# Kernel tuning notes

Hardware: AMD Instinct MI355X
Metric: run time of the kernel (lower is better)

## Reference

```python
import jax, jax.numpy as jnp
import numpy as np
from jax import lax

UNITS, FILTERS, KERNEL = 128, 32, 31
LSTM_SIZE = 1024


def _lstm_step(x, h, c, W, U, b):
    # Keras LSTMCell: gates ordered i, f, g(candidate), o
    z = x @ W + h @ U + b
    i, f, g, o = jnp.split(z, 4, axis=-1)
    c_new = jax.nn.sigmoid(f) * c + jax.nn.sigmoid(i) * jnp.tanh(g)
    h_new = jax.nn.sigmoid(o) * jnp.tanh(c_new)
    return h_new, c_new


def setup_inputs() -> dict:
    key = jax.random.key(0)
    ks = jax.random.split(key, 16)
    B, T_ENC, ENC_D = 32, 400, 512
    T_DEC, DEC_D = 800, 80
    s = 0.05
    inp = {
        "encoder_out_seq": jax.random.normal(ks[0], (B, T_ENC, ENC_D), jnp.float32),
        "decoder_out_seq": jax.random.normal(ks[1], (B, T_DEC, DEC_D), jnp.float32),
        # attention projections
        "Wm": jax.random.normal(ks[2], (ENC_D, UNITS), jnp.float32) * s,      # memory_layer
        "Wq": jax.random.normal(ks[3], (LSTM_SIZE, UNITS), jnp.float32) * s,  # query_layer
        "conv_k": jax.random.normal(ks[4], (KERNEL, 1, FILTERS), jnp.float32) * s,
        "conv_b": jnp.zeros((FILTERS,), jnp.float32),
        "Wloc": jax.random.normal(ks[5], (FILTERS, UNITS), jnp.float32) * s,  # location_layer
        "v_a": jax.random.normal(ks[6], (UNITS,), jnp.float32) * s,
        "b_a": jax.random.normal(ks[7], (UNITS,), jnp.float32) * s,
        # 2-layer decoder LSTM; layer0 input = dec_dim + enc_dim
        "W0": jax.random.normal(ks[8], (DEC_D + ENC_D, 4 * LSTM_SIZE), jnp.float32) * s,
        "U0": jax.random.normal(ks[9], (LSTM_SIZE, 4 * LSTM_SIZE), jnp.float32) * s,
        "b0": jnp.zeros((4 * LSTM_SIZE,), jnp.float32),
        "W1": jax.random.normal(ks[10], (LSTM_SIZE, 4 * LSTM_SIZE), jnp.float32) * s,
        "U1": jax.random.normal(ks[11], (LSTM_SIZE, 4 * LSTM_SIZE), jnp.float32) * s,
        "b1": jnp.zeros((4 * LSTM_SIZE,), jnp.float32),
    }
    return inp


def reference(encoder_out_seq, decoder_out_seq, Wm, Wq, conv_k, conv_b, Wloc,
              v_a, b_a, W0, U0, b0, W1, U1, b1):
    values = encoder_out_seq                      # [B, T_enc, D]
    keys = values @ Wm                            # [B, T_enc, units]
    B, T_enc, _ = values.shape

    def loc_conv(align):  # align: [B, T_enc]
        x = align[..., None]                      # [B, T_enc, 1]
        f = lax.conv_general_dilated(
            x, conv_k, window_strides=(1,), padding="SAME",
            dimension_numbers=("NWC", "WIO", "NWC"))
        return f + conv_b                         # [B, T_enc, filters]

    def step(carry, query):
        prev_align, c_i, h0, c0, h1, c1 = carry
        x = jnp.concatenate([query, c_i], axis=-1)           # [B, dec+enc]
        h0, c0 = _lstm_step(x, h0, c0, W0, U0, b0)
        h1, c1 = _lstm_step(h0, h1, c1, W1, U1, b1)
        pq = h1 @ Wq                                          # [B, units]
        loc = loc_conv(prev_align) @ Wloc                     # [B, T_enc, units]
        e = jnp.sum(v_a * jnp.tanh(keys + pq[:, None, :] + loc + b_a), axis=-1)
        a = jax.nn.softmax(e, axis=-1)                        # [B, T_enc]
        next_align = a + prev_align                           # cumulative
        c_new = jnp.einsum("bt,btd->bd", a, values)           # context
        return (next_align, c_new, h0, c0, h1, c1), a

    z = jnp.zeros
    init = (z((B, T_enc)), z((B, values.shape[-1])),
            z((B, LSTM_SIZE)), z((B, LSTM_SIZE)),
            z((B, LSTM_SIZE)), z((B, LSTM_SIZE)))
    queries = jnp.swapaxes(decoder_out_seq, 0, 1)             # [T_dec, B, dec_dim]
    _, e_tm = lax.scan(step, init, queries)                   # [T_dec, B, T_enc]
    e_outputs = jnp.swapaxes(e_tm, 0, 1)                      # [B, T_dec, T_enc]
    c_outputs = jnp.einsum("bqt,btd->bqd", e_outputs, values) # [B, T_dec, D]
    return c_outputs, e_outputs
```

## Files before the change

### kernel.cpp

```cpp
#include <hip/hip_runtime.h>
#include <hip/hip_bf16.h>
#include <math.h>
#include <stddef.h>

#define B   32
#define TE  400
#define TD  800
#define ED  512
#define DD  80
#define LS  1024
#define G4  4096
#define UN  128
#define FLT 32
#define KW  31
#define KSPLIT 16

__device__ __forceinline__ float fsig(float x){ return 1.f/(1.f+__expf(-x)); }
__device__ __forceinline__ float ftanh(float x){ return 1.f - 2.f/(__expf(2.f*x)+1.f); }

__global__ void keys_kernel(const float* __restrict__ values, const float* __restrict__ Wm,
                            float* __restrict__ keys)
{
    int b  = blockIdx.x;
    int tg = blockIdx.y;
    int tid = threadIdx.x;
    __shared__ __align__(16) float v[8*512];
    const float* vb = values + (size_t)b*TE*ED + (size_t)tg*8*ED;
    for (int i = tid; i < 8*512; i += 128) v[i] = vb[i];
    __syncthreads();
    int u = tid;
    float acc[8];
#pragma unroll
    for (int i=0;i<8;i++) acc[i]=0.f;
    for (int k=0;k<ED;k++){
        float w = Wm[k*UN + u];
#pragma unroll
        for (int tt=0; tt<8; tt++) acc[tt] += v[tt*512 + k]*w;
    }
#pragma unroll
    for (int tt=0; tt<8; tt++)
        keys[(size_t)b*TE*UN + (size_t)(tg*8+tt)*UN + u] = acc[tt];
}

__global__ void lstm_gemm_a(int t, const float* __restrict__ dec,
                            const float* __restrict__ c_out,
                            const float* __restrict__ h0,
                            const float* __restrict__ W0, const float* __restrict__ U0,
                            float* __restrict__ zbuf)
{
    const int KC = 101;
    int nx = blockIdx.x;
    int ky = blockIdx.y;
    int tid = threadIdx.x;
    int n  = nx*256 + tid;
    int k0 = ky*KC;
    __shared__ __align__(16) float xh[KC*32];
    for (int i = tid; i < KC*32; i += 256){
        int kk = i >> 5; int b = i & 31;
        int k = k0 + kk;
        float v;
        if (k < DD)           v = dec[(size_t)b*TD*DD + (size_t)t*DD + k];
        else if (k < DD+ED)   v = (t==0) ? 0.f
                                  : c_out[(size_t)b*TD*ED + (size_t)(t-1)*ED + (k-DD)];
        else                  v = h0[b*LS + (k-(DD+ED))];
        xh[i] = v;
    }
    __syncthreads();
    float acc[32];
#pragma unroll
    for (int i=0;i<32;i++) acc[i]=0.f;
    for (int kk=0; kk<KC; kk++){
        int k = k0 + kk;
        float w = (k < DD+ED) ? W0[(size_t)k*G4 + n]
                              : U0[(size_t)(k-(DD+ED))*G4 + n];
        const float4* xr = (const float4*)&xh[kk*32];
#pragma unroll
        for (int i=0;i<8;i++){
            float4 x4 = xr[i];
            acc[4*i+0] += x4.x*w;
            acc[4*i+1] += x4.y*w;
            acc[4*i+2] += x4.z*w;
            acc[4*i+3] += x4.w*w;
        }
    }
    float* zb = zbuf + (size_t)ky*B*G4;
#pragma unroll
    for (int b=0;b<32;b++) zb[b*G4 + n] = acc[b];
}

__global__ void lstm_gemm_b(const float* __restrict__ h0,
                            const float* __restrict__ h1,
                            const float* __restrict__ W1, const float* __restrict__ U1,
                            float* __restrict__ zbuf)
{
    const int KC = 128;
    int nx = blockIdx.x; int ky = blockIdx.y; int tid = threadIdx.x;
    int n  = nx*256 + tid;
    int k0 = ky*KC;
    __shared__ __align__(16) float xh[KC*32];
    for (int i = tid; i < KC*32; i += 256){
        int kk = i >> 5; int b = i & 31;
        int k = k0 + kk;
        xh[i] = (k < LS) ? h0[b*LS + k] : h1[b*LS + (k-LS)];
    }
    __syncthreads();
    float acc[32];
#pragma unroll
    for (int i=0;i<32;i++) acc[i]=0.f;
    for (int kk=0; kk<KC; kk++){
        int k = k0 + kk;
        float w = (k < LS) ? W1[(size_t)k*G4 + n] : U1[(size_t)(k-LS)*G4 + n];
        const float4* xr = (const float4*)&xh[kk*32];
#pragma unroll
        for (int i=0;i<8;i++){
            float4 x4 = xr[i];
            acc[4*i+0] += x4.x*w;
            acc[4*i+1] += x4.y*w;
            acc[4*i+2] += x4.z*w;
            acc[4*i+3] += x4.w*w;
        }
    }
    float* zb = zbuf + (size_t)ky*B*G4;
#pragma unroll
    for (int b=0;b<32;b++) zb[b*G4 + n] = acc[b];
}

__global__ void lstm_gate(const float* __restrict__ zbuf, const float* __restrict__ bias,
                          float* __restrict__ h, float* __restrict__ c,
                          float* __restrict__ denom)
{
    int idx = blockIdx.x*256 + threadIdx.x;
    int b = idx >> 10; int j = idx & 1023;
    float zs[4];
#pragma unroll
    for (int g=0; g<4; g++){
        int col = j + g*1024;
        float s = bias[col];
#pragma unroll
        for (int sp=0; sp<KSPLIT; sp++)
            s += zbuf[(size_t)sp*B*G4 + (size_t)b*G4 + col];
        zs[g] = s;
    }
    float cn = fsig(zs[1])*c[idx] + fsig(zs[0])*ftanh(zs[2]);
    float hn = fsig(zs[3])*ftanh(cn);
    c[idx] = cn; h[idx] = hn;
    if (denom != nullptr && idx < B) denom[idx] = 0.f;
}

__global__ void attn_energy(int t, const float* __restrict__ h1,
                            const float* __restrict__ Wq,
                            const float* __restrict__ keysb,
                            const float* __restrict__ align,
                            const float* __restrict__ convk, const float* __restrict__ convb,
                            const float* __restrict__ Wloc,
                            const float* __restrict__ v_a, const float* __restrict__ b_a,
                            float* __restrict__ e_out, float* __restrict__ denom)
{
    int chunk = blockIdx.x;
    int b = blockIdx.y;
    int t0 = chunk*50;
    int tid = threadIdx.x;
    __shared__ float pq[UN];
    __shared__ float aw[80];
    __shared__ float fls[50*FLT];
    __shared__ float elds[50*129];
    __shared__ float psum[50];

    if (tid < UN){
        int u = tid;
        float s = b_a[u];
        const float* hr = h1 + b*LS;
        for (int k=0; k<LS; k+=4){
            s += hr[k+0]*Wq[(k+0)*UN+u];
            s += hr[k+1]*Wq[(k+1)*UN+u];
            s += hr[k+2]*Wq[(k+2)*UN+u];
            s += hr[k+3]*Wq[(k+3)*UN+u];
        }
        pq[u] = s;
    } else if (tid < UN+80){
        int j = tid - UN;
        int p = t0 + j - 15;
        aw[j] = (p >= 0 && p < TE) ? align[b*TE + p] : 0.f;
    }
    __syncthreads();
    for (int o = tid; o < 50*FLT; o += 256){
        int pos = o >> 5, fl = o & 31;
        float s = convb[fl];
#pragma unroll
        for (int k=0; k<KW; k++) s += aw[pos+k]*convk[k*FLT + fl];
        fls[o] = s;
    }
    __syncthreads();
    const float* kb = keysb + (size_t)b*TE*UN + (size_t)t0*UN;
    for (int o = tid; o < 50*UN; o += 256){
        int pos = o >> 7, u = o & 127;
        float loc = 0.f;
        const float* fr = &fls[pos*FLT];
#pragma unroll
        for (int fl=0; fl<FLT; fl++) loc += fr[fl]*Wloc[fl*UN + u];
        float x = kb[pos*UN + u] + pq[u] + loc;
        elds[pos*129 + u] = v_a[u]*ftanh(x);
    }
    __syncthreads();
    if (tid < 50){
        int pos = tid;
        float e = 0.f;
        for (int u=0; u<UN; u++) e += elds[pos*129 + u];
        float ex = __expf(e);
        e_out[(size_t)b*TD*TE + (size_t)t*TE + t0 + pos] = ex;
        psum[pos] = ex;
    }
    __syncthreads();
    if (tid == 0){
        float s = 0.f;
        for (int p=0; p<50; p++) s += psum[p];
        atomicAdd(&denom[b], s);
    }
}

__global__ void attn_ctx(int t, const float* __restrict__ values,
                         const float* __restrict__ denom,
                         float* __restrict__ e_out, float* __restrict__ align,
                         float* __restrict__ c_out)
{
    int chunk = blockIdx.x; int b = blockIdx.y;
    int t0 = chunk*50; int tid = threadIdx.x;
    __shared__ float alds[50];
    if (tid < 50){
        size_t ei = (size_t)b*TD*TE + (size_t)t*TE + t0 + tid;
        float a = e_out[ei] / denom[b];
        e_out[ei] = a;
        align[b*TE + t0 + tid] += a;
        alds[tid] = a;
    }
    __syncthreads();
    const float* vb = values + (size_t)b*TE*ED + (size_t)t0*ED;
    float* cr = c_out + (size_t)b*TD*ED + (size_t)t*ED;
    for (int d = tid; d < ED; d += 256){
        float acc = 0.f;
#pragma unroll 10
        for (int p=0; p<50; p++) acc += alds[p]*vb[p*ED + d];
        atomicAdd(&cr[d], acc);
    }
}

extern "C" void kernel_launch(void* const* d_in, const int* in_sizes, int n_in,
                              void* d_out, int out_size, void* d_ws, size_t ws_size,
                              hipStream_t stream)
{
    const float* enc   = (const float*)d_in[0];
    const float* dec   = (const float*)d_in[1];
    const float* Wm    = (const float*)d_in[2];
    const float* Wq    = (const float*)d_in[3];
    const float* convk = (const float*)d_in[4];
    const float* convb = (const float*)d_in[5];
    const float* Wloc  = (const float*)d_in[6];
    const float* v_a   = (const float*)d_in[7];
    const float* b_a   = (const float*)d_in[8];
    const float* W0    = (const float*)d_in[9];
    const float* U0    = (const float*)d_in[10];
    const float* b0    = (const float*)d_in[11];
    const float* W1    = (const float*)d_in[12];
    const float* U1    = (const float*)d_in[13];
    const float* b1    = (const float*)d_in[14];

    float* out   = (float*)d_out;
    float* c_out = out;
    float* e_out = out + (size_t)B*TD*ED;

    float* ws    = (float*)d_ws;
    float* h0    = ws;
    float* c0    = h0 + B*LS;
    float* h1    = c0 + B*LS;
    float* c1    = h1 + B*LS;
    float* align = c1 + B*LS;
    float* denom = align + B*TE;
    float* keys  = denom + B;
    float* zbuf0 = keys  + (size_t)B*TE*UN;
    float* zbuf1 = zbuf0 + (size_t)KSPLIT*B*G4;

    hipMemsetAsync(ws, 0, (size_t)(4*B*LS + B*TE + B)*sizeof(float), stream);
    hipMemsetAsync(c_out, 0, (size_t)B*TD*ED*sizeof(float), stream);

    keys_kernel<<<dim3(B,50), 128, 0, stream>>>(enc, Wm, keys);

    for (int t=0; t<TD; t++){
        lstm_gemm_a<<<dim3(16,16), 256, 0, stream>>>(t, dec, c_out, h0, W0, U0, zbuf0);
        lstm_gate  <<<128, 256, 0, stream>>>(zbuf0, b0, h0, c0, denom);
        lstm_gemm_b<<<dim3(16,16), 256, 0, stream>>>(h0, h1, W1, U1, zbuf1);
        lstm_gate  <<<128, 256, 0, stream>>>(zbuf1, b1, h1, c1, nullptr);
        attn_energy<<<dim3(8,B), 256, 0, stream>>>(t, h1, Wq, keys, align,
                                                   convk, convb, Wloc, v_a, b_a,
                                                   e_out, denom);
        attn_ctx   <<<dim3(8,B), 256, 0, stream>>>(t, enc, denom, e_out, align, c_out);
    }
}
```

Baseline: 106.4 ms.

## Replace per-step kernel launches with a persistent kernel using grid barriers

The 4800 small per-timestep launches are replaced by one persistent kernel of 256 blocks. Each decoder step runs the LSTM layers and attention phases separated by software grid barriers. Each block keeps its LSTM cell state in shared memory and owns a fixed slice of gate columns and batch rows. Softmax normalization is deferred: context partials and unnormalized exponentials are stored, then fixed up in separate normalization kernels after the loop. The intent is to remove launch overhead and global partial-sum buffers, at the risk of deadlock if all 256 blocks cannot be co-resident, plus the cost of barrier spinning.

```diff
diff --git a/kernel.cpp b/kernel.cpp
--- a/kernel.cpp
+++ b/kernel.cpp
@@ -1,5 +1,4 @@
 #include <hip/hip_runtime.h>
-#include <hip/hip_bf16.h>
 #include <math.h>
 #include <stddef.h>
 
@@ -13,7 +12,9 @@
 #define UN  128
 #define FLT 32
 #define KW  31
-#define KSPLIT 16
+
+#define NBLK 256
+#define NTHR 512
 
 __device__ __forceinline__ float fsig(float x){ return 1.f/(1.f+__expf(-x)); }
 __device__ __forceinline__ float ftanh(float x){ return 1.f - 2.f/(__expf(2.f*x)+1.f); }
@@ -42,206 +43,318 @@
         keys[(size_t)b*TE*UN + (size_t)(tg*8+tt)*UN + u] = acc[tt];
 }
 
-__global__ void lstm_gemm_a(int t, const float* __restrict__ dec,
-                            const float* __restrict__ c_out,
-                            const float* __restrict__ h0,
-                            const float* __restrict__ W0, const float* __restrict__ U0,
-                            float* __restrict__ zbuf)
-{
-    const int KC = 101;
-    int nx = blockIdx.x;
-    int ky = blockIdx.y;
-    int tid = threadIdx.x;
-    int n  = nx*256 + tid;
-    int k0 = ky*KC;
-    __shared__ __align__(16) float xh[KC*32];
-    for (int i = tid; i < KC*32; i += 256){
-        int kk = i >> 5; int b = i & 31;
-        int k = k0 + kk;
-        float v;
-        if (k < DD)           v = dec[(size_t)b*TD*DD + (size_t)t*DD + k];
-        else if (k < DD+ED)   v = (t==0) ? 0.f
-                                  : c_out[(size_t)b*TD*ED + (size_t)(t-1)*ED + (k-DD)];
-        else                  v = h0[b*LS + (k-(DD+ED))];
-        xh[i] = v;
+__global__ void dect_kernel(const float* __restrict__ dec, float* __restrict__ decT)
+{
+    int t = blockIdx.x; int tid = threadIdx.x;
+    __shared__ float tile[32*80];
+    for (int o = tid; o < 32*80; o += 256){
+        int b = o/80, k = o%80;
+        tile[o] = dec[((size_t)b*TD + t)*DD + k];
     }
     __syncthreads();
-    float acc[32];
-#pragma unroll
-    for (int i=0;i<32;i++) acc[i]=0.f;
-    for (int kk=0; kk<KC; kk++){
-        int k = k0 + kk;
-        float w = (k < DD+ED) ? W0[(size_t)k*G4 + n]
-                              : U0[(size_t)(k-(DD+ED))*G4 + n];
-        const float4* xr = (const float4*)&xh[kk*32];
-#pragma unroll
-        for (int i=0;i<8;i++){
-            float4 x4 = xr[i];
-            acc[4*i+0] += x4.x*w;
-            acc[4*i+1] += x4.y*w;
-            acc[4*i+2] += x4.z*w;
-            acc[4*i+3] += x4.w*w;
-        }
+    for (int o = tid; o < 80*32; o += 256){
+        int k = o>>5, b = o&31;
+        decT[((size_t)t*DD + k)*B + b] = tile[b*80 + k];
     }
-    float* zb = zbuf + (size_t)ky*B*G4;
-#pragma unroll
-    for (int b=0;b<32;b++) zb[b*G4 + n] = acc[b];
-}
-
-__global__ void lstm_gemm_b(const float* __restrict__ h0,
-                            const float* __restrict__ h1,
-                            const float* __restrict__ W1, const float* __restrict__ U1,
-                            float* __restrict__ zbuf)
-{
-    const int KC = 128;
-    int nx = blockIdx.x; int ky = blockIdx.y; int tid = threadIdx.x;
-    int n  = nx*256 + tid;
-    int k0 = ky*KC;
-    __shared__ __align__(16) float xh[KC*32];
-    for (int i = tid; i < KC*32; i += 256){
-        int kk = i >> 5; int b = i & 31;
-        int k = k0 + kk;
-        xh[i] = (k < LS) ? h0[b*LS + k] : h1[b*LS + (k-LS)];
+}
+
+__device__ __forceinline__ void gridbar(unsigned* cnt, unsigned* gen, unsigned& epoch)
+{
+    __syncthreads();
+    if (threadIdx.x == 0){
+        epoch++;
+        unsigned prev = __hip_atomic_fetch_add(cnt, 1u, __ATOMIC_ACQ_REL, __HIP_MEMORY_SCOPE_AGENT);
+        if (prev == (unsigned)(NBLK-1)){
+            __hip_atomic_store(cnt, 0u, __ATOMIC_RELAXED, __HIP_MEMORY_SCOPE_AGENT);
+            __hip_atomic_store(gen, epoch, __ATOMIC_RELEASE, __HIP_MEMORY_SCOPE_AGENT);
+        } else {
+            while (__hip_atomic_load(gen, __ATOMIC_RELAXED, __HIP_MEMORY_SCOPE_AGENT) < epoch)
+                __builtin_amdgcn_s_sleep(2);
+            (void)__hip_atomic_load(gen, __ATOMIC_ACQUIRE, __HIP_MEMORY_SCOPE_AGENT);
+        }
     }
     __syncthreads();
-    float acc[32];
-#pragma unroll
-    for (int i=0;i<32;i++) acc[i]=0.f;
-    for (int kk=0; kk<KC; kk++){
-        int k = k0 + kk;
-        float w = (k < LS) ? W1[(size_t)k*G4 + n] : U1[(size_t)(k-LS)*G4 + n];
-        const float4* xr = (const float4*)&xh[kk*32];
-#pragma unroll
-        for (int i=0;i<8;i++){
-            float4 x4 = xr[i];
-            acc[4*i+0] += x4.x*w;
-            acc[4*i+1] += x4.y*w;
-            acc[4*i+2] += x4.z*w;
-            acc[4*i+3] += x4.w*w;
-        }
+}
+
+__global__ __launch_bounds__(NTHR, 2) void persist(
+    const float* __restrict__ enc,
+    const float* __restrict__ decT,
+    const float* __restrict__ keys,
+    const float* __restrict__ W0, const float* __restrict__ U0, const float* __restrict__ b0v,
+    const float* __restrict__ W1, const float* __restrict__ U1, const float* __restrict__ b1v,
+    const float* __restrict__ Wq, const float* __restrict__ convk, const float* __restrict__ convb,
+    const float* __restrict__ Wloc, const float* __restrict__ v_a, const float* __restrict__ b_a,
+    float* __restrict__ h0T,
+    float* __restrict__ h1T,
+    float* __restrict__ align_,
+    float* __restrict__ denomh,
+    float* __restrict__ ctxp,
+    unsigned* __restrict__ bar,
+    float* __restrict__ c_out, float* __restrict__ e_out)
+{
+    __shared__ __align__(16) float xh[512*16];
+    __shared__ float zp[512*17];
+    __shared__ float zr[512];
+    __shared__ float cst0[128], cst1[128];
+    __shared__ float invd[16];
+    __shared__ float pqp[512];
+    __shared__ float pq[128];
+    __shared__ float aw[96];
+    __shared__ float fls[50*FLT];
+    __shared__ float epart[128];
+    __shared__ float alds[64];
+    __shared__ float wtile[32*33];
+
+    const int tid = threadIdx.x;
+    const int p   = blockIdx.x;
+    const int xcd  = p & 7, slot = p >> 3;
+    const int ut   = xcd*16 + (slot>>1);
+    const int bt   = slot & 1;
+    const int b0   = bt*16;
+    const int c    = tid & 31;
+    const int ks   = tid >> 5;
+    const int gate = c >> 3, ui = c & 7;
+    const int col  = gate*1024 + ut*8 + ui;
+    const int ab  = p >> 3;
+    const int ach = p & 7;
+    const int t0  = ach*50;
+
+    if (tid < 128){ cst0[tid] = 0.f; cst1[tid] = 0.f; }
+    unsigned epoch = 0;
+    unsigned* cntp = bar;
+    unsigned* genp = bar + 32;
+    __syncthreads();
+
+    for (int t = 0; t < TD; t++){
+        if (tid < 16) invd[tid] = (t==0) ? 0.f : 1.f/denomh[(size_t)(t-1)*B + b0 + tid];
+        __syncthreads();
+        {
+            float acc[16];
+#pragma unroll
+            for (int i=0;i<16;i++) acc[i]=0.f;
+            const float* wA = W0 + col;
+            const float* wB = U0 + col;
+            for (int k0 = 0; k0 < 1616; k0 += 404){
+                for (int i = tid; i < 404*16; i += NTHR){
+                    int kk = i >> 4, bb = i & 15;
+                    int k = k0 + kk;
+                    float v;
+                    if (k < DD) v = decT[((size_t)t*DD + k)*B + b0 + bb];
+                    else if (k < DD+ED){
+                        if (t == 0) v = 0.f;
+                        else {
+                            int d = k - DD;
+                            float s8 = 0.f;
+#pragma unroll
+                            for (int ch=0; ch<8; ch++) s8 += ctxp[((size_t)ch*ED + d)*B + b0 + bb];
+                            v = s8 * invd[bb];
+                        }
+                    } else v = h0T[(size_t)((t&1)^1)*LS*B + (size_t)(k-(DD+ED))*B + b0 + bb];
+                    xh[i] = v;
+                }
+                __syncthreads();
+                for (int kk = ks; kk < 404; kk += 16){
+                    int k = k0 + kk;
+                    float w = (k < DD+ED) ? wA[(size_t)k*G4] : wB[(size_t)(k-(DD+ED))*G4];
+                    const float4* xr = (const float4*)&xh[kk*16];
+#pragma unroll
+                    for (int i=0;i<4;i++){
+                        float4 x4 = xr[i];
+                        acc[4*i+0] += x4.x*w; acc[4*i+1] += x4.y*w;
+                        acc[4*i+2] += x4.z*w; acc[4*i+3] += x4.w*w;
+                    }
+                }
+                __syncthreads();
+            }
+#pragma unroll
+            for (int bb=0; bb<16; bb++) zp[(ks*32 + c)*17 + bb] = acc[bb];
+        }
+        __syncthreads();
+        {
+            int co = tid >> 4, bb = tid & 15;
+            float z = 0.f;
+#pragma unroll
+            for (int q=0;q<16;q++) z += zp[(q*32 + co)*17 + bb];
+            zr[tid] = z + b0v[(co>>3)*1024 + ut*8 + (co&7)];
+        }
+        __syncthreads();
+        if (tid < 128){
+            int uio = tid >> 4, bb = tid & 15;
+            float zi = zr[(0*8+uio)*16 + bb];
+            float zf = zr[(1*8+uio)*16 + bb];
+            float zg = zr[(2*8+uio)*16 + bb];
+            float zo = zr[(3*8+uio)*16 + bb];
+            float cn = fsig(zf)*cst0[tid] + fsig(zi)*ftanh(zg);
+            float hn = fsig(zo)*ftanh(cn);
+            cst0[tid] = cn;
+            h0T[(size_t)(t&1)*LS*B + (size_t)(ut*8+uio)*B + b0 + bb] = hn;
+        }
+        if (p < 16 && t > 0){
+            int d0 = p*32;
+            for (int o = tid; o < 1024; o += NTHR){
+                int dd = o>>5, bb = o&31;
+                float s8 = 0.f;
+#pragma unroll
+                for (int ch=0; ch<8; ch++) s8 += ctxp[((size_t)ch*ED + d0+dd)*B + bb];
+                wtile[dd*33+bb] = s8;
+            }
+            __syncthreads();
+            for (int o = tid; o < 1024; o += NTHR){
+                int bb = o>>5, dd = o&31;
+                c_out[((size_t)bb*TD + (t-1))*ED + d0+dd] = wtile[dd*33+bb];
+            }
+        }
+        gridbar(cntp, genp, epoch);
+
+        if (t > 0 && tid < 50){
+            float idn = 1.f / denomh[(size_t)(t-1)*B + ab];
+            align_[(size_t)ab*TE + t0 + tid] +=
+                e_out[((size_t)ab*TD + (t-1))*TE + t0 + tid] * idn;
+        }
+        {
+            float acc[16];
+#pragma unroll
+            for (int i=0;i<16;i++) acc[i]=0.f;
+            const float* wA = W1 + col;
+            const float* wB = U1 + col;
+            for (int k0 = 0; k0 < 2048; k0 += 512){
+                for (int i = tid; i < 512*16; i += NTHR){
+                    int kk = i >> 4, bb = i & 15;
+                    int k = k0 + kk;
+                    xh[i] = (k < LS) ? h0T[(size_t)(t&1)*LS*B + (size_t)k*B + b0 + bb]
+                                     : h1T[(size_t)((t&1)^1)*LS*B + (size_t)(k-LS)*B + b0 + bb];
+                }
+                __syncthreads();
+                for (int kk = ks; kk < 512; kk += 16){
+                    int k = k0 + kk;
+                    float w = (k < LS) ? wA[(size_t)k*G4] : wB[(size_t)(k-LS)*G4];
+                    const float4* xr = (const float4*)&xh[kk*16];
+#pragma unroll
+                    for (int i=0;i<4;i++){
+                        float4 x4 = xr[i];
+                        acc[4*i+0] += x4.x*w; acc[4*i+1] += x4.y*w;
+                        acc[4*i+2] += x4.z*w; acc[4*i+3] += x4.w*w;
+                    }
+                }
+                __syncthreads();
+            }
+#pragma unroll
+            for (int bb=0; bb<16; bb++) zp[(ks*32 + c)*17 + bb] = acc[bb];
+        }
+        __syncthreads();
+        {
+            int co = tid >> 4, bb = tid & 15;
+            float z = 0.f;
+#pragma unroll
+            for (int q=0;q<16;q++) z += zp[(q*32 + co)*17 + bb];
+            zr[tid] = z + b1v[(co>>3)*1024 + ut*8 + (co&7)];
+        }
+        __syncthreads();
+        if (tid < 128){
+            int uio = tid >> 4, bb = tid & 15;
+            float zi = zr[(0*8+uio)*16 + bb];
+            float zf = zr[(1*8+uio)*16 + bb];
+            float zg = zr[(2*8+uio)*16 + bb];
+            float zo = zr[(3*8+uio)*16 + bb];
+            float cn = fsig(zf)*cst1[tid] + fsig(zi)*ftanh(zg);
+            float hn = fsig(zo)*ftanh(cn);
+            cst1[tid] = cn;
+            h1T[(size_t)(t&1)*LS*B + (size_t)(ut*8+uio)*B + b0 + bb] = hn;
+        }
+        gridbar(cntp, genp, epoch);
+
+        {
+            const float* h1r = h1T + (size_t)(t&1)*LS*B;
+            int u = tid & 127, kq = tid >> 7;
+            float s = 0.f;
+            for (int k = kq*256; k < kq*256+256; k++)
+                s += h1r[(size_t)k*B + ab] * Wq[(size_t)k*UN + u];
+            pqp[kq*128 + u] = s;
+        }
+        if (tid >= 128 && tid < 208){
+            int j = tid - 128;
+            int pp = t0 + j - 15;
+            aw[j] = (pp >= 0 && pp < TE) ? align_[(size_t)ab*TE + pp] : 0.f;
+        }
+        __syncthreads();
+        if (tid < 128) pq[tid] = pqp[tid] + pqp[128+tid] + pqp[256+tid] + pqp[384+tid] + b_a[tid];
+        __syncthreads();
+        for (int o = tid; o < 50*FLT; o += NTHR){
+            int pos = o >> 5, fl = o & 31;
+            float s = convb[fl];
+#pragma unroll
+            for (int k=0;k<KW;k++) s += aw[pos+k]*convk[k*FLT+fl];
+            fls[o] = s;
+        }
+        __syncthreads();
+        {
+            const float* kb = keys + ((size_t)ab*TE + t0)*UN;
+            for (int o = tid; o < 50*UN; o += NTHR){
+                int pos = o >> 7, u = o & 127;
+                float loc = 0.f;
+                const float* fr = &fls[pos*FLT];
+#pragma unroll
+                for (int fl=0; fl<FLT; fl++) loc += fr[fl]*Wloc[fl*UN+u];
+                float x = kb[(size_t)pos*UN + u] + pq[u] + loc;
+                float val = v_a[u]*ftanh(x);
+                val += __shfl_down(val, 32, 64);
+                val += __shfl_down(val, 16, 64);
+                val += __shfl_down(val,  8, 64);
+                val += __shfl_down(val,  4, 64);
+                val += __shfl_down(val,  2, 64);
+                val += __shfl_down(val,  1, 64);
+                if ((tid & 63) == 0) epart[o >> 6] = val;
+            }
+        }
+        __syncthreads();
+        if (tid < 50){
+            float e = epart[tid*2] + epart[tid*2+1];
+            float ex = __expf(e);
+            e_out[((size_t)ab*TD + t)*TE + t0 + tid] = ex;
+            alds[tid] = ex;
+        }
+        __syncthreads();
+        if (tid == 0){
+            float s = 0.f;
+#pragma unroll
+            for (int i=0;i<50;i++) s += alds[i];
+            atomicAdd(&denomh[(size_t)t*B + ab], s);
+        }
+        {
+            const float* vb = enc + ((size_t)ab*TE + t0)*ED;
+            float a2 = 0.f;
+#pragma unroll 10
+            for (int pp=0; pp<50; pp++) a2 += alds[pp]*vb[(size_t)pp*ED + tid];
+            ctxp[((size_t)ach*ED + tid)*B + ab] = a2;
+        }
+        gridbar(cntp, genp, epoch);
     }
-    float* zb = zbuf + (size_t)ky*B*G4;
-#pragma unroll
-    for (int b=0;b<32;b++) zb[b*G4 + n] = acc[b];
-}
-
-__global__ void lstm_gate(const float* __restrict__ zbuf, const float* __restrict__ bias,
-                          float* __restrict__ h, float* __restrict__ c,
-                          float* __restrict__ denom)
-{
-    int idx = blockIdx.x*256 + threadIdx.x;
-    int b = idx >> 10; int j = idx & 1023;
-    float zs[4];
-#pragma unroll
-    for (int g=0; g<4; g++){
-        int col = j + g*1024;
-        float s = bias[col];
-#pragma unroll
-        for (int sp=0; sp<KSPLIT; sp++)
-            s += zbuf[(size_t)sp*B*G4 + (size_t)b*G4 + col];
-        zs[g] = s;
-    }
-    float cn = fsig(zs[1])*c[idx] + fsig(zs[0])*ftanh(zs[2]);
-    float hn = fsig(zs[3])*ftanh(cn);
-    c[idx] = cn; h[idx] = hn;
-    if (denom != nullptr && idx < B) denom[idx] = 0.f;
-}
-
-__global__ void attn_energy(int t, const float* __restrict__ h1,
-                            const float* __restrict__ Wq,
-                            const float* __restrict__ keysb,
-                            const float* __restrict__ align,
-                            const float* __restrict__ convk, const float* __restrict__ convb,
-                            const float* __restrict__ Wloc,
-                            const float* __restrict__ v_a, const float* __restrict__ b_a,
-                            float* __restrict__ e_out, float* __restrict__ denom)
-{
-    int chunk = blockIdx.x;
-    int b = blockIdx.y;
-    int t0 = chunk*50;
-    int tid = threadIdx.x;
-    __shared__ float pq[UN];
-    __shared__ float aw[80];
-    __shared__ float fls[50*FLT];
-    __shared__ float elds[50*129];
-    __shared__ float psum[50];
-
-    if (tid < UN){
-        int u = tid;
-        float s = b_a[u];
-        const float* hr = h1 + b*LS;
-        for (int k=0; k<LS; k+=4){
-            s += hr[k+0]*Wq[(k+0)*UN+u];
-            s += hr[k+1]*Wq[(k+1)*UN+u];
-            s += hr[k+2]*Wq[(k+2)*UN+u];
-            s += hr[k+3]*Wq[(k+3)*UN+u];
-        }
-        pq[u] = s;
-    } else if (tid < UN+80){
-        int j = tid - UN;
-        int p = t0 + j - 15;
-        aw[j] = (p >= 0 && p < TE) ? align[b*TE + p] : 0.f;
-    }
-    __syncthreads();
-    for (int o = tid; o < 50*FLT; o += 256){
-        int pos = o >> 5, fl = o & 31;
-        float s = convb[fl];
-#pragma unroll
-        for (int k=0; k<KW; k++) s += aw[pos+k]*convk[k*FLT + fl];
-        fls[o] = s;
-    }
-    __syncthreads();
-    const float* kb = keysb + (size_t)b*TE*UN + (size_t)t0*UN;
-    for (int o = tid; o < 50*UN; o += 256){
-        int pos = o >> 7, u = o & 127;
-        float loc = 0.f;
-        const float* fr = &fls[pos*FLT];
-#pragma unroll
-        for (int fl=0; fl<FLT; fl++) loc += fr[fl]*Wloc[fl*UN + u];
-        float x = kb[pos*UN + u] + pq[u] + loc;
-        elds[pos*129 + u] = v_a[u]*ftanh(x);
-    }
-    __syncthreads();
-    if (tid < 50){
-        int pos = tid;
-        float e = 0.f;
-        for (int u=0; u<UN; u++) e += elds[pos*129 + u];
-        float ex = __expf(e);
-        e_out[(size_t)b*TD*TE + (size_t)t*TE + t0 + pos] = ex;
-        psum[pos] = ex;
-    }
-    __syncthreads();
-    if (tid == 0){
-        float s = 0.f;
-        for (int p=0; p<50; p++) s += psum[p];
-        atomicAdd(&denom[b], s);
-    }
-}
-
-__global__ void attn_ctx(int t, const float* __restrict__ values,
-                         const float* __restrict__ denom,
-                         float* __restrict__ e_out, float* __restrict__ align,
-                         float* __restrict__ c_out)
-{
-    int chunk = blockIdx.x; int b = blockIdx.y;
-    int t0 = chunk*50; int tid = threadIdx.x;
-    __shared__ float alds[50];
-    if (tid < 50){
-        size_t ei = (size_t)b*TD*TE + (size_t)t*TE + t0 + tid;
-        float a = e_out[ei] / denom[b];
-        e_out[ei] = a;
-        align[b*TE + t0 + tid] += a;
-        alds[tid] = a;
-    }
-    __syncthreads();
-    const float* vb = values + (size_t)b*TE*ED + (size_t)t0*ED;
-    float* cr = c_out + (size_t)b*TD*ED + (size_t)t*ED;
-    for (int d = tid; d < ED; d += 256){
-        float acc = 0.f;
-#pragma unroll 10
-        for (int p=0; p<50; p++) acc += alds[p]*vb[p*ED + d];
-        atomicAdd(&cr[d], acc);
-    }
+}
+
+__global__ void norm_e_kernel(const float* __restrict__ denomh, float* __restrict__ e_out)
+{
+    size_t idx = (size_t)blockIdx.x*512 + threadIdx.x;
+    int b = (int)(idx / ((size_t)TD*TE));
+    int r = (int)(idx % ((size_t)TD*TE));
+    int t = r / TE;
+    e_out[idx] = e_out[idx] / denomh[(size_t)t*B + b];
+}
+
+__global__ void norm_c_kernel(const float* __restrict__ denomh, const float* __restrict__ ctxp,
+                              float* __restrict__ c_out)
+{
+    size_t idx = (size_t)blockIdx.x*512 + threadIdx.x;
+    int b = (int)(idx / ((size_t)TD*ED));
+    int r = (int)(idx % ((size_t)TD*ED));
+    int t = r / ED;
+    int d = r % ED;
+    float v;
+    if (t == TD-1){
+        v = 0.f;
+#pragma unroll
+        for (int ch=0; ch<8; ch++) v += ctxp[((size_t)ch*ED + d)*B + b];
+    } else v = c_out[idx];
+    c_out[idx] = v / denomh[(size_t)t*B + b];
 }
 
 extern "C" void kernel_launch(void* const* d_in, const int* in_sizes, int n_in,
@@ -268,30 +381,28 @@
     float* c_out = out;
     float* e_out = out + (size_t)B*TD*ED;
 
-    float* ws    = (float*)d_ws;
-    float* h0    = ws;
-    float* c0    = h0 + B*LS;
-    float* h1    = c0 + B*LS;
-    float* c1    = h1 + B*LS;
-    float* align = c1 + B*LS;
-    float* denom = align + B*TE;
-    float* keys  = denom + B;
-    float* zbuf0 = keys  + (size_t)B*TE*UN;
-    float* zbuf1 = zbuf0 + (size_t)KSPLIT*B*G4;
-
-    hipMemsetAsync(ws, 0, (size_t)(4*B*LS + B*TE + B)*sizeof(float), stream);
-    hipMemsetAsync(c_out, 0, (size_t)B*TD*ED*sizeof(float), stream);
+    float* ws     = (float*)d_ws;
+    float* h0T    = ws;
+    float* h1T    = h0T + (size_t)2*LS*B;
+    float* align_ = h1T + (size_t)2*LS*B;
+    float* denomh = align_ + (size_t)B*TE;
+    unsigned* bar = (unsigned*)(denomh + (size_t)TD*B);
+    float* keys   = denomh + (size_t)TD*B + 64;
+    float* decT   = keys + (size_t)B*TE*UN;
+    float* ctxp   = decT + (size_t)TD*DD*B;
+
+    hipMemsetAsync(ws, 0,
+        ((size_t)(4*LS*B + B*TE + TD*B) + 64)*sizeof(float), stream);
 
     keys_kernel<<<dim3(B,50), 128, 0, stream>>>(enc, Wm, keys);
-
-    for (int t=0; t<TD; t++){
-        lstm_gemm_a<<<dim3(16,16), 256, 0, stream>>>(t, dec, c_out, h0, W0, U0, zbuf0);
-        lstm_gate  <<<128, 256, 0, stream>>>(zbuf0, b0, h0, c0, denom);
-        lstm_gemm_b<<<dim3(16,16), 256, 0, stream>>>(h0, h1, W1, U1, zbuf1);
-        lstm_gate  <<<128, 256, 0, stream>>>(zbuf1, b1, h1, c1, nullptr);
-        attn_energy<<<dim3(8,B), 256, 0, stream>>>(t, h1, Wq, keys, align,
-                                                   convk, convb, Wloc, v_a, b_a,
-                                                   e_out, denom);
-        attn_ctx   <<<dim3(8,B), 256, 0, stream>>>(t, enc, denom, e_out, align, c_out);
-    }
-}
+    dect_kernel<<<TD, 256, 0, stream>>>(dec, decT);
+
+    persist<<<NBLK, NTHR, 0, stream>>>(enc, decT, keys,
+                                       W0, U0, b0, W1, U1, b1,
+                                       Wq, convk, convb, Wloc, v_a, b_a,
+                                       h0T, h1T, align_, denomh, ctxp, bar,
+                                       c_out, e_out);
+
+    norm_e_kernel<<<(B*TD*TE)/512, 512, 0, stream>>>(denomh, e_out);
+    norm_c_kernel<<<(B*TD*ED)/512, 512, 0, stream>>>(denomh, ctxp, c_out);
+}
```

Result: slower. 176.8 ms (+66.1%).
